# Kernel tuning notes

Measured on AMD Instinct MI355X. Metric: run time of the kernel, lower is better.

Reference implementation:

```python
import jax, jax.numpy as jnp
import numpy as np

B, C, L, K = 64, 2, 131072, 4


def setup_inputs() -> dict:
    key = jax.random.key(0)
    k1, k2, k3, k4 = jax.random.split(key, 4)
    x = jax.random.normal(k1, (B, C, L), dtype=jnp.float32)
    Bs = 0.5 * jax.random.normal(k2, (B, C, K, 3), dtype=jnp.float32)
    # Build stable denominators: complex-conjugate poles r*exp(+-j*theta), r < 0.95
    # a(z) = 1 - 2 r cos(theta) z^-1 + r^2 z^-2  -> guaranteed-stable IIR cascade.
    r = jax.random.uniform(k3, (B, C, K), minval=0.1, maxval=0.95)
    theta = jax.random.uniform(k4, (B, C, K), minval=0.05, maxval=np.pi - 0.05)
    a1 = -2.0 * r * jnp.cos(theta)
    a2 = r * r
    As = jnp.stack([jnp.ones_like(a1), a1, a2], axis=-1).astype(jnp.float32)
    return {"input_signal": x, "Bs": Bs, "As": As}


def _biquad_cascade(x, b, a):
    # x: [N, L]; b, a: [N, K, 3] with a already normalized (a0 == 1).
    # Serial cascade of K biquads, each in direct form II transposed:
    #   y[n]  = b0*u[n] + s1
    #   s1'   = b1*u[n] - a1*y[n] + s2
    #   s2'   = b2*u[n] - a2*y[n]
    # Exactly the linear recurrence the ssm/lfilter backends compute.
    nK = b.shape[1]
    b0, b1, b2 = b[..., 0], b[..., 1], b[..., 2]  # each [N, K]
    a1, a2 = a[..., 1], a[..., 2]

    def step(carry, xt):
        s1, s2 = carry  # each [N, K]
        u = xt  # [N]
        s1n, s2n = [], []
        for k in range(nK):  # small fixed cascade depth, unrolled
            y = b0[:, k] * u + s1[:, k]
            s1n.append(b1[:, k] * u - a1[:, k] * y + s2[:, k])
            s2n.append(b2[:, k] * u - a2[:, k] * y)
            u = y
        return (jnp.stack(s1n, axis=1), jnp.stack(s2n, axis=1)), u

    N = x.shape[0]
    init = (jnp.zeros((N, nK), x.dtype), jnp.zeros((N, nK), x.dtype))
    _, ys = jax.lax.scan(step, init, x.T)  # scan over time: ys [L, N]
    return ys.T


def reference(input_signal, Bs, As):
    b, c, audio_len = input_signal.shape
    assert Bs.shape[-1] == As.shape[-1] == 3
    # channel broadcasting as in _process_ssm
    if c == 1 and Bs.shape[1] > 1:
        input_signal = jnp.broadcast_to(input_signal, (b, Bs.shape[1], audio_len))
        c = Bs.shape[1]
    elif Bs.shape[1] == 1 and c > 1:
        Bs = jnp.broadcast_to(Bs, (b, c) + Bs.shape[2:])
        As = jnp.broadcast_to(As, (b, c) + As.shape[2:])
    a0 = As[..., :1]
    Bn = (Bs / a0).reshape(b * c, -1, 3)
    An = (As / a0).reshape(b * c, -1, 3)
    x = input_signal.reshape(b * c, audio_len)
    y = _biquad_cascade(x, Bn, An)
    return y.reshape(b, c, audio_len)
```

## Files before the change

kernel.cpp:

```cpp
#include <hip/hip_runtime.h>
#include <math.h>


#define SS   64
#define WMAX 384
#define WMIN 64
#define TT   32
#define TPB  256
#define LSTR 33
#define KB   4

typedef float vf4 __attribute__((ext_vector_type(4)));

__global__ void iir_prep_kernel(const float* __restrict__ As, int rows,
                                int* __restrict__ wrow, int* __restrict__ perm)
{
    __shared__ int sw[256];
    const int r = threadIdx.x;
    int W = 0;
    if (r < rows) {
        float r2max = 0.f;
#pragma unroll
        for (int k = 0; k < KB; ++k) {
            float a0 = As[(size_t)r * KB * 3 + 3 * k];
            float a2 = As[(size_t)r * KB * 3 + 3 * k + 2] / a0;
            r2max = fmaxf(r2max, a2);
        }
        float rmax = fminf(fmaxf(sqrtf(fmaxf(r2max, 0.f)), 0.20f), 0.955f);
        float Wf = 25.6f / (-logf(rmax));
        W = ((int)ceilf(Wf) + TT - 1) & ~(TT - 1);
        W = min(max(W, WMIN), WMAX);
        wrow[r] = W;
    }
    sw[r] = W;
    __syncthreads();
    if (r < rows) {
        int rank = 0;
        for (int i = 0; i < rows; ++i)
            rank += (sw[i] > W) || (sw[i] == W && i < r);
        perm[rank] = r;
    }
}

__global__ __launch_bounds__(TPB) void iir_chunks_kernel(
    const float* __restrict__ x, const float* __restrict__ Bs,
    const float* __restrict__ As, float* __restrict__ out, int L,
    const int* __restrict__ wrow, const int* __restrict__ perm)
{
    __shared__ float lds[TPB * LSTR];
    const int tid = threadIdx.x;
    const int bpr = (L / SS) / TPB;
    const int row = perm[blockIdx.x / bpr];
    const int chunk0 = (blockIdx.x % bpr) * TPB;
    const int W = wrow[row];

    float b0[KB], b1[KB], b2[KB], na1[KB], na2[KB];
    const float* Bp = Bs + (size_t)row * KB * 3;
    const float* Ap = As + (size_t)row * KB * 3;
#pragma unroll
    for (int k = 0; k < KB; ++k) {
        float inv = 1.0f / Ap[3 * k];
        b0[k]  =  Bp[3 * k]     * inv;
        b1[k]  =  Bp[3 * k + 1] * inv;
        b2[k]  =  Bp[3 * k + 2] * inv;
        na1[k] = -Ap[3 * k + 1] * inv;
        na2[k] = -Ap[3 * k + 2] * inv;
    }

    float s1[KB] = {0.f, 0.f, 0.f, 0.f};
    float s2[KB] = {0.f, 0.f, 0.f, 0.f};

    const float* xrow = x   + (size_t)row * L;
    float*       orow = out + (size_t)row * L;
    float*       myrow = lds + tid * LSTR;

    const int NT = (SS + W) / TT;
    const int WT = W / TT;

#pragma unroll 1
    for (int it = 0; it < NT; ++it) {
        const int i0 = it * TT - W;

#pragma unroll
        for (int l = 0; l < (TPB * TT / 4) / TPB; ++l) {
            int e  = l * TPB + tid;
            int j  = e >> 3;
            int p4 = (e & 7) << 2;
            int pos = (chunk0 + j) * SS + i0 + p4;
            float4 v = make_float4(0.f, 0.f, 0.f, 0.f);
            if (pos >= 0) v = *reinterpret_cast<const float4*>(xrow + pos);
            float* d = lds + j * LSTR + p4;
            d[0] = v.x; d[1] = v.y; d[2] = v.z; d[3] = v.w;
        }
        __syncthreads();

        if (it < WT) {
#pragma unroll
            for (int p = 0; p < TT; ++p) {
                float u = myrow[p];
#pragma unroll
                for (int k = 0; k < KB; ++k) {
                    float yv = fmaf(b0[k], u, s1[k]);
                    s1[k] = fmaf(na1[k], yv, fmaf(b1[k], u, s2[k]));
                    s2[k] = fmaf(na2[k], yv, b2[k] * u);
                    u = yv;
                }
            }
            __syncthreads();
        } else {
#pragma unroll
            for (int p = 0; p < TT; ++p) {
                float u = myrow[p];
#pragma unroll
                for (int k = 0; k < KB; ++k) {
                    float yv = fmaf(b0[k], u, s1[k]);
                    s1[k] = fmaf(na1[k], yv, fmaf(b1[k], u, s2[k]));
                    s2[k] = fmaf(na2[k], yv, b2[k] * u);
                    u = yv;
                }
                myrow[p] = u;
            }
            __syncthreads();

#pragma unroll
            for (int l = 0; l < 8; ++l) {
                int e  = l * TPB + tid;
                int j  = e >> 3;
                int p4 = (e & 7) << 2;
                int pos = (chunk0 + j) * SS + i0 + p4;
                const float* sp = lds + j * LSTR + p4;
                vf4 v = { sp[0], sp[1], sp[2], sp[3] };
                __builtin_nontemporal_store(v, reinterpret_cast<vf4*>(orow + pos));
            }
            __syncthreads();
        }
    }
}

extern "C" void kernel_launch(void* const* d_in, const int* in_sizes, int n_in,
                              void* d_out, int out_size, void* d_ws, size_t ws_size,
                              hipStream_t stream) {
    const float* x  = (const float*)d_in[0];
    const float* Bs = (const float*)d_in[1];
    const float* As = (const float*)d_in[2];
    float* out = (float*)d_out;

    const int rows = in_sizes[1] / (KB * 3);
    const int L    = in_sizes[0] / rows;
    const int bpr  = (L / SS) / TPB;

    int* wrow = (int*)d_ws;
    int* perm = wrow + rows;

    hipLaunchKernelGGL(iir_prep_kernel, dim3(1), dim3(256), 0, stream,
                       As, rows, wrow, perm);
    hipLaunchKernelGGL(iir_chunks_kernel, dim3(rows * bpr), dim3(TPB), 0, stream,
                       x, Bs, As, out, L, wrow, perm);
}
```

Baseline: 156.8 us.

## Prefetch next input tile into registers to overlap global loads with recurrence

Loads the next time tile of input into registers while the current tile is processed, so the global load latency is overlapped with the serial biquad compute. Per-thread offsets are precomputed once, and the sync structure is reorganized: one barrier at the loop top replaces the trailing barriers. Launch bounds now request 4 blocks per SM, which may limit registers given the extra 32 prefetch registers and risk spills.

```diff
diff --git a/kernel.cpp b/kernel.cpp
--- a/kernel.cpp
+++ b/kernel.cpp
@@ -9,6 +9,7 @@
 #define TPB  256
 #define LSTR 33
 #define KB   4
+#define NL   8
 
 typedef float vf4 __attribute__((ext_vector_type(4)));
 
@@ -42,7 +43,7 @@
     }
 }
 
-__global__ __launch_bounds__(TPB) void iir_chunks_kernel(
+__global__ __launch_bounds__(TPB, 4) void iir_chunks_kernel(
     const float* __restrict__ x, const float* __restrict__ Bs,
     const float* __restrict__ As, float* __restrict__ out, int L,
     const int* __restrict__ wrow, const int* __restrict__ perm)
@@ -74,24 +75,48 @@
     float*       orow = out + (size_t)row * L;
     float*       myrow = lds + tid * LSTR;
 
+    const int tq = tid >> 3;
+    const int p4 = (tid & 7) << 2;
+    int off[NL];
+    int ldsoff[NL];
+#pragma unroll
+    for (int l = 0; l < NL; ++l) {
+        int j = l * 32 + tq;
+        off[l]    = (chunk0 + j) * SS + p4 - W;
+        ldsoff[l] = j * LSTR + p4;
+    }
+
     const int NT = (SS + W) / TT;
     const int WT = W / TT;
 
+    float4 rn[NL];
+#pragma unroll
+    for (int l = 0; l < NL; ++l) {
+        int pos = off[l];
+        rn[l] = make_float4(0.f, 0.f, 0.f, 0.f);
+        if (pos >= 0) rn[l] = *reinterpret_cast<const float4*>(xrow + pos);
+    }
+
 #pragma unroll 1
     for (int it = 0; it < NT; ++it) {
-        const int i0 = it * TT - W;
+        __syncthreads();
 
 #pragma unroll
-        for (int l = 0; l < (TPB * TT / 4) / TPB; ++l) {
-            int e  = l * TPB + tid;
-            int j  = e >> 3;
-            int p4 = (e & 7) << 2;
-            int pos = (chunk0 + j) * SS + i0 + p4;
-            float4 v = make_float4(0.f, 0.f, 0.f, 0.f);
-            if (pos >= 0) v = *reinterpret_cast<const float4*>(xrow + pos);
-            float* d = lds + j * LSTR + p4;
-            d[0] = v.x; d[1] = v.y; d[2] = v.z; d[3] = v.w;
+        for (int l = 0; l < NL; ++l) {
+            float* d = lds + ldsoff[l];
+            d[0] = rn[l].x; d[1] = rn[l].y; d[2] = rn[l].z; d[3] = rn[l].w;
         }
+
+        if (it + 1 < NT) {
+            const int base = (it + 1) * TT;
+#pragma unroll
+            for (int l = 0; l < NL; ++l) {
+                int pos = off[l] + base;
+                rn[l] = make_float4(0.f, 0.f, 0.f, 0.f);
+                if (pos >= 0) rn[l] = *reinterpret_cast<const float4*>(xrow + pos);
+            }
+        }
+
         __syncthreads();
 
         if (it < WT) {
@@ -106,7 +131,6 @@
                     u = yv;
                 }
             }
-            __syncthreads();
         } else {
 #pragma unroll
             for (int p = 0; p < TT; ++p) {
@@ -122,17 +146,14 @@
             }
             __syncthreads();
 
+            const int base = it * TT - W;
 #pragma unroll
-            for (int l = 0; l < 8; ++l) {
-                int e  = l * TPB + tid;
-                int j  = e >> 3;
-                int p4 = (e & 7) << 2;
-                int pos = (chunk0 + j) * SS + i0 + p4;
-                const float* sp = lds + j * LSTR + p4;
+            for (int l = 0; l < NL; ++l) {
+                const float* sp = lds + ldsoff[l];
                 vf4 v = { sp[0], sp[1], sp[2], sp[3] };
-                __builtin_nontemporal_store(v, reinterpret_cast<vf4*>(orow + pos));
+                __builtin_nontemporal_store(
+                    v, reinterpret_cast<vf4*>(orow + off[l] + W + base));
             }
-            __syncthreads();
         }
     }
 }
```

Result: faster. 141.3 us (-9.9%).
